# Kernel tuning notes

Measured on AMD Instinct MI355X. Metric: run time of the kernel, lower is better.

The kernel has to match this reference:

```python
import jax, jax.numpy as jnp
import numpy as np

N_NODES = 100000
N_EDGES = 1600000
D = 128


def setup_inputs() -> dict:
    key = jax.random.key(0)
    ks = jax.random.split(key, 10)
    features = jax.random.normal(ks[0], (N_NODES, D), dtype=jnp.float32)
    edge_index = jax.random.randint(ks[1], (2, N_EDGES), 0, N_NODES, dtype=jnp.int64)
    edge_weight = jax.random.uniform(ks[2], (N_EDGES,), dtype=jnp.float32)
    scale = 1.0 / np.sqrt(D)
    W1 = jax.random.normal(ks[3], (D, D), dtype=jnp.float32) * scale
    b1 = jnp.zeros((D,), dtype=jnp.float32)
    a1 = jnp.full((D,), 0.25, dtype=jnp.float32)  # PReLU init
    W2 = jax.random.normal(ks[4], (D, D), dtype=jnp.float32) * scale
    b2 = jnp.zeros((D,), dtype=jnp.float32)
    a2 = jnp.full((D,), 0.25, dtype=jnp.float32)
    return {"features": features, "edge_index": edge_index, "edge_weight": edge_weight,
            "W1": W1, "b1": b1, "a1": a1, "W2": W2, "b2": b2, "a2": a2}


def _gcn_norm(edge_index, edge_weight, n_nodes):
    # PyG GCNConv default: add self-loops (weight 1), symmetric normalization.
    src, dst = edge_index[0], edge_index[1]
    loop = jnp.arange(n_nodes, dtype=src.dtype)
    src = jnp.concatenate([src, loop])
    dst = jnp.concatenate([dst, loop])
    w = jnp.concatenate([edge_weight, jnp.ones((n_nodes,), edge_weight.dtype)])
    deg = jax.ops.segment_sum(w, dst, num_segments=n_nodes)  # in-degree (target)
    dis = jnp.where(deg > 0, jax.lax.rsqrt(deg), 0.0)
    norm = dis[src] * w * dis[dst]  # [E + N]
    return src, dst, norm


def _gcn_layer(x, W, b, src, dst, norm, n_nodes):
    h = x @ W                                 # [N, D] dense GEMM first (PyG order)
    msg = h[src] * norm[:, None]              # gather + scale, [E+N, D]
    out = jax.ops.segment_sum(msg, dst, num_segments=n_nodes)
    return out + b


def _prelu(x, a):
    return jnp.where(x >= 0, x, a * x)


def reference(features, edge_index, edge_weight, W1, b1, a1, W2, b2, a2):
    n = features.shape[0]
    src, dst, norm = _gcn_norm(edge_index, edge_weight, n)
    # dropout is identity in eval mode
    x = _prelu(_gcn_layer(features, W1, b1, src, dst, norm, n), a1)
    x = _prelu(_gcn_layer(x, W2, b2, src, dst, norm, n), a2)
    return x
```

## Files before the change

kernel.cpp:

```cpp
#include <hip/hip_runtime.h>
#include <cstdint>

#define NN 100000
#define NE 1600000
#define DD 128
#define NB 250
#define BSZ 400

typedef unsigned int uint;
typedef unsigned short ushort;
typedef unsigned long long u64;

typedef __attribute__((ext_vector_type(8))) short short8;
typedef __attribute__((ext_vector_type(4))) float floatx4;

__device__ inline uint f2bf(float f) {
    uint u = __float_as_uint(f);
    return (u + 0x7fffu + ((u >> 16) & 1u)) >> 16;
}


__global__ __launch_bounds__(256) void zero_bc(uint* __restrict__ bc) {
    if (threadIdx.x < NB) bc[threadIdx.x] = 0u;
}

__global__ __launch_bounds__(256) void bucket_hist(const int* __restrict__ dst,
                                                   uint* __restrict__ bc) {
    __shared__ uint h[NB];
    int tid = threadIdx.x;
    if (tid < NB) h[tid] = 0u;
    __syncthreads();
    int e0 = blockIdx.x * 8192 + tid;
#pragma unroll
    for (int k = 0; k < 32; ++k) {
        int e = e0 + 256 * k;
        if (e < NE) atomicAdd(&h[(uint)dst[e] / BSZ], 1u);
    }
    __syncthreads();
    if (tid < NB && h[tid]) atomicAdd(&bc[tid], h[tid]);
}

__global__ __launch_bounds__(256) void bucket_prefix(const uint* __restrict__ bc,
                                                     uint* __restrict__ bbase,
                                                     uint* __restrict__ bcur) {
    int lane = threadIdx.x;
    if (lane < 64) {
        uint v[4], s = 0;
#pragma unroll
        for (int k = 0; k < 4; ++k) {
            int i = lane * 4 + k;
            v[k] = (i < NB) ? bc[i] : 0u;
            s += v[k];
        }
        uint inc = s;
#pragma unroll
        for (int d = 1; d < 64; d <<= 1) {
            uint t = __shfl_up(inc, (unsigned)d, 64);
            if (lane >= d) inc += t;
        }
        uint run = inc - s;
#pragma unroll
        for (int k = 0; k < 4; ++k) {
            int i = lane * 4 + k;
            if (i < NB) { bbase[i] = run; bcur[i] = run; run += v[k]; }
        }
        if (lane == 63) bbase[NB] = run;
    }
}

__global__ __launch_bounds__(256) void bucket_append(const int* __restrict__ src,
                                                     const int* __restrict__ dst,
                                                     const float* __restrict__ w,
                                                     uint* __restrict__ bcur,
                                                     int2* __restrict__ etmp) {
    __shared__ uint h[NB];
    __shared__ uint res[NB];
    int tid = threadIdx.x;
    if (tid < NB) h[tid] = 0u;
    __syncthreads();
    int e0 = blockIdx.x * 4096 + tid;
    uint rank[16], bkt[16];
#pragma unroll
    for (int k = 0; k < 16; ++k) {
        int e = e0 + 256 * k;
        if (e < NE) {
            uint b = (uint)dst[e] / BSZ;
            bkt[k] = b;
            rank[k] = atomicAdd(&h[b], 1u);
        } else bkt[k] = 0xffffffffu;
    }
    __syncthreads();
    if (tid < NB) res[tid] = h[tid] ? atomicAdd(&bcur[tid], h[tid]) : 0u;
    __syncthreads();
#pragma unroll
    for (int k = 0; k < 16; ++k) {
        if (bkt[k] != 0xffffffffu) {
            int e = e0 + 256 * k;
            uint dl = (uint)dst[e] - bkt[k] * BSZ;
            uint wq = (uint)(w[e] * 8388608.0f);
            if (wq > 8388607u) wq = 8388607u;
            etmp[res[bkt[k]] + rank[k]] = make_int2(src[e], (int)((dl << 23) | wq));
        }
    }
}

__global__ __launch_bounds__(256) void bucket_build(const int2* __restrict__ etmp,
                                                    const uint* __restrict__ bbase,
                                                    float* __restrict__ dis,
                                                    int* __restrict__ hist_g,
                                                    int* __restrict__ rowstart,
                                                    int2* __restrict__ edges) {
    __shared__ u64   wc[BSZ];
    __shared__ uint  cur[BSZ];
    __shared__ float disl[BSZ];
    int tid = threadIdx.x;
    int b = blockIdx.x;
    int n0 = b * BSZ;
    for (int i = tid; i < BSZ; i += 256) wc[i] = 0ull;
    __syncthreads();
    uint base = bbase[b], end = bbase[b + 1];
    for (uint i = base + tid; i < end; i += 256) {
        uint y = (uint)etmp[i].y;
        uint dl = y >> 23;
        atomicAdd(&wc[dl], ((u64)1 << 40) | (u64)(y & 0x7fffffu));
    }
    __syncthreads();
    if (tid < 64) {
        uint v[7], s = 0;
#pragma unroll
        for (int k = 0; k < 7; ++k) {
            int i = tid * 7 + k;
            v[k] = (i < BSZ) ? (uint)(wc[i] >> 40) : 0u;
            s += v[k];
        }
        uint inc = s;
#pragma unroll
        for (int d = 1; d < 64; d <<= 1) {
            uint t = __shfl_up(inc, (unsigned)d, 64);
            if (tid >= d) inc += t;
        }
        uint run = inc - s;
#pragma unroll
        for (int k = 0; k < 7; ++k) {
            int i = tid * 7 + k;
            if (i < BSZ) { cur[i] = run; run += v[k]; }
        }
    }
    __syncthreads();
    for (int i = tid; i < BSZ; i += 256) {
        u64 v = wc[i];
        float wsum = (float)(v & 0xffffffffffull) * (1.0f / 8388608.0f);
        float ds = rsqrtf(1.0f + wsum);
        disl[i] = ds;
        dis[n0 + i] = ds;
        hist_g[n0 + i] = (int)(v >> 40);
        rowstart[n0 + i] = (int)(base + cur[i]);
    }
    __syncthreads();
    for (uint i = base + tid; i < end; i += 256) {
        int2 e = etmp[i];
        uint y = (uint)e.y;
        uint dl = y >> 23;
        float wv = (float)(y & 0x7fffffu) * (1.0f / 8388608.0f);
        uint p = atomicAdd(&cur[dl], 1u);
        float nrm = wv * disl[dl];
        edges[base + p] = make_int2(e.x, __float_as_int(nrm));
    }
}

#define WTS 136
#define NTILES ((NN + 63) / 64)

template <bool AF32>
__global__ __launch_bounds__(256) void gemm_mfma(const void* __restrict__ Xv,
                                                 const float* __restrict__ W,
                                                 const float* __restrict__ dis,
                                                 ushort* __restrict__ HB) {
    __shared__ ushort Wt[DD * WTS];
    int tid = threadIdx.x;
#pragma unroll
    for (int it = 0; it < 16; ++it) {
        int flat = (tid + it * 256) * 4;
        int k = flat >> 7, n = flat & 127;
        float4 wv = *(const float4*)&W[flat];
        Wt[(n + 0) * WTS + k] = (ushort)f2bf(wv.x);
        Wt[(n + 1) * WTS + k] = (ushort)f2bf(wv.y);
        Wt[(n + 2) * WTS + k] = (ushort)f2bf(wv.z);
        Wt[(n + 3) * WTS + k] = (ushort)f2bf(wv.w);
    }
    __syncthreads();

    int wave = tid >> 6, lane = tid & 63;
    int q = lane >> 4, l16 = lane & 15;

    for (int tile = blockIdx.x; tile < NTILES; tile += gridDim.x) {
        int row0 = tile * 64 + wave * 16;

        int arow = row0 + l16;
        if (arow >= NN) arow = NN - 1;
        short8 afr[4];
        if (AF32) {
            const float* xr = (const float*)Xv + (size_t)arow * DD + q * 8;
#pragma unroll
            for (int ks = 0; ks < 4; ++ks) {
                float4 f0 = *(const float4*)(xr + ks * 32);
                float4 f1 = *(const float4*)(xr + ks * 32 + 4);
                uint4 u;
                u.x = f2bf(f0.x) | (f2bf(f0.y) << 16);
                u.y = f2bf(f0.z) | (f2bf(f0.w) << 16);
                u.z = f2bf(f1.x) | (f2bf(f1.y) << 16);
                u.w = f2bf(f1.z) | (f2bf(f1.w) << 16);
                afr[ks] = __builtin_bit_cast(short8, u);
            }
        } else {
            const ushort* xr = (const ushort*)Xv + (size_t)arow * DD + q * 8;
#pragma unroll
            for (int ks = 0; ks < 4; ++ks)
                afr[ks] = *(const short8*)(xr + ks * 32);
        }

        floatx4 acc[8];
#pragma unroll
        for (int ct = 0; ct < 8; ++ct) acc[ct] = (floatx4)(0.0f);

#pragma unroll
        for (int ct = 0; ct < 8; ++ct) {
            const ushort* wp = &Wt[(ct * 16 + l16) * WTS + q * 8];
#pragma unroll
            for (int ks = 0; ks < 4; ++ks) {
                short8 bfr = *(const short8*)(wp + ks * 32);
                acc[ct] = __builtin_amdgcn_mfma_f32_16x16x32_bf16(afr[ks], bfr, acc[ct], 0, 0, 0);
            }
        }

#pragma unroll
        for (int reg = 0; reg < 4; ++reg) {
            int r = row0 + q * 4 + reg;
            if (r < NN) {
                float ds = dis[r];
                ushort* orow = HB + (size_t)r * DD + l16;
#pragma unroll
                for (int ct = 0; ct < 8; ++ct)
                    orow[ct * 16] = (ushort)f2bf(acc[ct][reg] * ds);
            }
        }
    }
}

__device__ inline float4 bf4(uint2 u) {
    float4 f;
    f.x = __uint_as_float(u.x << 16);
    f.y = __uint_as_float(u.x & 0xffff0000u);
    f.z = __uint_as_float(u.y << 16);
    f.w = __uint_as_float(u.y & 0xffff0000u);
    return f;
}

template <bool BF16OUT>
__global__ __launch_bounds__(256) void gather_finalize(const ushort* __restrict__ hb,
                                                       const int2* __restrict__ edges,
                                                       const int* __restrict__ rowstart,
                                                       const int* __restrict__ hist,
                                                       const float* __restrict__ dis,
                                                       const float* __restrict__ b,
                                                       const float* __restrict__ a,
                                                       void* __restrict__ xout) {
    int tid = threadIdx.x;
    int lane = tid & 31;
    int node = blockIdx.x * 8 + (tid >> 5);

    const int2* ep = edges + rowstart[node];
    int cnt = hist[node];
    float ds = dis[node];

    const uint2* hrow = (const uint2*)(hb + (size_t)node * DD) + lane;
    float4 self = bf4(*hrow);
    float4 acc0, acc1, acc2, acc3;
    acc0.x = self.x * ds; acc0.y = self.y * ds;
    acc0.z = self.z * ds; acc0.w = self.w * ds;
    acc1 = make_float4(0.f, 0.f, 0.f, 0.f);
    acc2 = make_float4(0.f, 0.f, 0.f, 0.f);
    acc3 = make_float4(0.f, 0.f, 0.f, 0.f);

    int j = 0;
    for (; j + 8 <= cnt; j += 8) {
        int2 e0 = ep[j];     int2 e1 = ep[j + 1];
        int2 e2 = ep[j + 2]; int2 e3 = ep[j + 3];
        int2 e4 = ep[j + 4]; int2 e5 = ep[j + 5];
        int2 e6 = ep[j + 6]; int2 e7 = ep[j + 7];
        uint2 u0 = *((const uint2*)(hb + (size_t)e0.x * DD) + lane);
        uint2 u1 = *((const uint2*)(hb + (size_t)e1.x * DD) + lane);
        uint2 u2 = *((const uint2*)(hb + (size_t)e2.x * DD) + lane);
        uint2 u3 = *((const uint2*)(hb + (size_t)e3.x * DD) + lane);
        uint2 u4 = *((const uint2*)(hb + (size_t)e4.x * DD) + lane);
        uint2 u5 = *((const uint2*)(hb + (size_t)e5.x * DD) + lane);
        uint2 u6 = *((const uint2*)(hb + (size_t)e6.x * DD) + lane);
        uint2 u7 = *((const uint2*)(hb + (size_t)e7.x * DD) + lane);
        float n0 = __int_as_float(e0.y), n1 = __int_as_float(e1.y);
        float n2 = __int_as_float(e2.y), n3 = __int_as_float(e3.y);
        float n4 = __int_as_float(e4.y), n5 = __int_as_float(e5.y);
        float n6 = __int_as_float(e6.y), n7 = __int_as_float(e7.y);
        float4 v0 = bf4(u0), v1 = bf4(u1), v2 = bf4(u2), v3 = bf4(u3);
        float4 v4 = bf4(u4), v5 = bf4(u5), v6 = bf4(u6), v7 = bf4(u7);
        acc0.x += v0.x * n0; acc0.y += v0.y * n0; acc0.z += v0.z * n0; acc0.w += v0.w * n0;
        acc1.x += v1.x * n1; acc1.y += v1.y * n1; acc1.z += v1.z * n1; acc1.w += v1.w * n1;
        acc2.x += v2.x * n2; acc2.y += v2.y * n2; acc2.z += v2.z * n2; acc2.w += v2.w * n2;
        acc3.x += v3.x * n3; acc3.y += v3.y * n3; acc3.z += v3.z * n3; acc3.w += v3.w * n3;
        acc0.x += v4.x * n4; acc0.y += v4.y * n4; acc0.z += v4.z * n4; acc0.w += v4.w * n4;
        acc1.x += v5.x * n5; acc1.y += v5.y * n5; acc1.z += v5.z * n5; acc1.w += v5.w * n5;
        acc2.x += v6.x * n6; acc2.y += v6.y * n6; acc2.z += v6.z * n6; acc2.w += v6.w * n6;
        acc3.x += v7.x * n7; acc3.y += v7.y * n7; acc3.z += v7.z * n7; acc3.w += v7.w * n7;
    }
    for (; j < cnt; ++j) {
        int2 e = ep[j];
        uint2 u = *((const uint2*)(hb + (size_t)e.x * DD) + lane);
        float n = __int_as_float(e.y);
        float4 v = bf4(u);
        acc0.x += v.x * n; acc0.y += v.y * n; acc0.z += v.z * n; acc0.w += v.w * n;
    }

    float4 bb = ((const float4*)b)[lane];
    float4 aa = ((const float4*)a)[lane];
    float4 r;
    r.x = acc0.x + acc1.x + acc2.x + acc3.x + bb.x;
    r.y = acc0.y + acc1.y + acc2.y + acc3.y + bb.y;
    r.z = acc0.z + acc1.z + acc2.z + acc3.z + bb.z;
    r.w = acc0.w + acc1.w + acc2.w + acc3.w + bb.w;
    r.x = r.x >= 0.f ? r.x : aa.x * r.x;
    r.y = r.y >= 0.f ? r.y : aa.y * r.y;
    r.z = r.z >= 0.f ? r.z : aa.z * r.z;
    r.w = r.w >= 0.f ? r.w : aa.w * r.w;
    if (BF16OUT) {
        uint2 o;
        o.x = f2bf(r.x) | (f2bf(r.y) << 16);
        o.y = f2bf(r.z) | (f2bf(r.w) << 16);
        ((uint2*)xout)[(size_t)node * 32 + lane] = o;
    } else {
        ((float4*)xout)[(size_t)node * 32 + lane] = r;
    }
}

extern "C" void kernel_launch(void* const* d_in, const int* in_sizes, int n_in,
                              void* d_out, int out_size, void* d_ws, size_t ws_size,
                              hipStream_t stream) {
    const float* feat = (const float*)d_in[0];
    const int*   ei   = (const int*)d_in[1];
    const float* ew   = (const float*)d_in[2];
    const float* W1   = (const float*)d_in[3];
    const float* b1   = (const float*)d_in[4];
    const float* a1   = (const float*)d_in[5];
    const float* W2   = (const float*)d_in[6];
    const float* b2   = (const float*)d_in[7];
    const float* a2   = (const float*)d_in[8];
    float* out = (float*)d_out;

    const int* srcp = ei;
    const int* dstp = ei + NE;

    char* wsb = (char*)d_ws;
    size_t off = 0;
    uint* bc     = (uint*)(wsb + off); off += 4096;
    uint* bbase  = (uint*)(wsb + off); off += 4096;
    uint* bcur   = (uint*)(wsb + off); off += 4096;
    float* dis   = (float*)(wsb + off); off += 4ull * NN;
    int* hist    = (int*)(wsb + off); off += 4ull * NN;
    int* rowstart= (int*)(wsb + off); off += 4ull * NN;
    int2* etmp   = (int2*)(wsb + off); off += 8ull * NE;
    int2* edges  = (int2*)(wsb + off); off += 8ull * NE;
    ushort* hb   = (ushort*)(wsb + off); off += 2ull * NN * DD;
    ushort* x1b  = (ushort*)(wsb + off); off += 2ull * NN * DD;

    zero_bc<<<1, 256, 0, stream>>>(bc);
    bucket_hist<<<(NE + 8191) / 8192, 256, 0, stream>>>(dstp, bc);
    bucket_prefix<<<1, 256, 0, stream>>>(bc, bbase, bcur);
    bucket_append<<<(NE + 4095) / 4096, 256, 0, stream>>>(srcp, dstp, ew, bcur, etmp);
    bucket_build<<<NB, 256, 0, stream>>>(etmp, bbase, dis, hist, rowstart, edges);

    const int gemm_blocks = (NTILES + 1) / 2;
    const int gath_blocks = NN / 8;

    gemm_mfma<true><<<gemm_blocks, 256, 0, stream>>>(feat, W1, dis, hb);
    gather_finalize<true><<<gath_blocks, 256, 0, stream>>>(hb, edges, rowstart, hist, dis, b1, a1, x1b);
    gemm_mfma<false><<<gemm_blocks, 256, 0, stream>>>(x1b, W2, dis, hb);
    gather_finalize<false><<<gath_blocks, 256, 0, stream>>>(hb, edges, rowstart, hist, dis, b2, a2, out);
}
```

Measured before the change: 379.0 us.

## Gather with one wavefront per node and lane-broadcast edge lists

Restructures the gather/finalize kernel so each node is handled by a full 64-lane wavefront that reads 4 bytes (two bf16 values) per lane, instead of a half-wave of 32 lanes reading 8 bytes each. Edge records are loaded 16 at a time, one per lane, and broadcast with readlane, so the per-edge index loads become scalar and the next chunk is prefetched. The aim is to cut redundant per-lane edge loads and raise memory-level parallelism in the bandwidth-bound gather. In exchange, each row gather is narrower per lane, twice as many blocks are launched, and tail iterations do masked dummy loads of row 0.

```diff
diff --git a/kernel.cpp b/kernel.cpp
--- a/kernel.cpp
+++ b/kernel.cpp
@@ -247,15 +247,6 @@
     }
 }
 
-__device__ inline float4 bf4(uint2 u) {
-    float4 f;
-    f.x = __uint_as_float(u.x << 16);
-    f.y = __uint_as_float(u.x & 0xffff0000u);
-    f.z = __uint_as_float(u.y << 16);
-    f.w = __uint_as_float(u.y & 0xffff0000u);
-    return f;
-}
-
 template <bool BF16OUT>
 __global__ __launch_bounds__(256) void gather_finalize(const ushort* __restrict__ hb,
                                                        const int2* __restrict__ edges,
@@ -265,78 +256,54 @@
                                                        const float* __restrict__ b,
                                                        const float* __restrict__ a,
                                                        void* __restrict__ xout) {
-    int tid = threadIdx.x;
-    int lane = tid & 31;
-    int node = blockIdx.x * 8 + (tid >> 5);
-
-    const int2* ep = edges + rowstart[node];
-    int cnt = hist[node];
+    int node = blockIdx.x * 4 + (threadIdx.x >> 6);
+    int lane = threadIdx.x & 63;
+
+    int rs  = __builtin_amdgcn_readfirstlane(rowstart[node]);
+    int cnt = __builtin_amdgcn_readfirstlane(hist[node]);
     float ds = dis[node];
-
-    const uint2* hrow = (const uint2*)(hb + (size_t)node * DD) + lane;
-    float4 self = bf4(*hrow);
-    float4 acc0, acc1, acc2, acc3;
-    acc0.x = self.x * ds; acc0.y = self.y * ds;
-    acc0.z = self.z * ds; acc0.w = self.w * ds;
-    acc1 = make_float4(0.f, 0.f, 0.f, 0.f);
-    acc2 = make_float4(0.f, 0.f, 0.f, 0.f);
-    acc3 = make_float4(0.f, 0.f, 0.f, 0.f);
-
-    int j = 0;
-    for (; j + 8 <= cnt; j += 8) {
-        int2 e0 = ep[j];     int2 e1 = ep[j + 1];
-        int2 e2 = ep[j + 2]; int2 e3 = ep[j + 3];
-        int2 e4 = ep[j + 4]; int2 e5 = ep[j + 5];
-        int2 e6 = ep[j + 6]; int2 e7 = ep[j + 7];
-        uint2 u0 = *((const uint2*)(hb + (size_t)e0.x * DD) + lane);
-        uint2 u1 = *((const uint2*)(hb + (size_t)e1.x * DD) + lane);
-        uint2 u2 = *((const uint2*)(hb + (size_t)e2.x * DD) + lane);
-        uint2 u3 = *((const uint2*)(hb + (size_t)e3.x * DD) + lane);
-        uint2 u4 = *((const uint2*)(hb + (size_t)e4.x * DD) + lane);
-        uint2 u5 = *((const uint2*)(hb + (size_t)e5.x * DD) + lane);
-        uint2 u6 = *((const uint2*)(hb + (size_t)e6.x * DD) + lane);
-        uint2 u7 = *((const uint2*)(hb + (size_t)e7.x * DD) + lane);
-        float n0 = __int_as_float(e0.y), n1 = __int_as_float(e1.y);
-        float n2 = __int_as_float(e2.y), n3 = __int_as_float(e3.y);
-        float n4 = __int_as_float(e4.y), n5 = __int_as_float(e5.y);
-        float n6 = __int_as_float(e6.y), n7 = __int_as_float(e7.y);
-        float4 v0 = bf4(u0), v1 = bf4(u1), v2 = bf4(u2), v3 = bf4(u3);
-        float4 v4 = bf4(u4), v5 = bf4(u5), v6 = bf4(u6), v7 = bf4(u7);
-        acc0.x += v0.x * n0; acc0.y += v0.y * n0; acc0.z += v0.z * n0; acc0.w += v0.w * n0;
-        acc1.x += v1.x * n1; acc1.y += v1.y * n1; acc1.z += v1.z * n1; acc1.w += v1.w * n1;
-        acc2.x += v2.x * n2; acc2.y += v2.y * n2; acc2.z += v2.z * n2; acc2.w += v2.w * n2;
-        acc3.x += v3.x * n3; acc3.y += v3.y * n3; acc3.z += v3.z * n3; acc3.w += v3.w * n3;
-        acc0.x += v4.x * n4; acc0.y += v4.y * n4; acc0.z += v4.z * n4; acc0.w += v4.w * n4;
-        acc1.x += v5.x * n5; acc1.y += v5.y * n5; acc1.z += v5.z * n5; acc1.w += v5.w * n5;
-        acc2.x += v6.x * n6; acc2.y += v6.y * n6; acc2.z += v6.z * n6; acc2.w += v6.w * n6;
-        acc3.x += v7.x * n7; acc3.y += v7.y * n7; acc3.z += v7.z * n7; acc3.w += v7.w * n7;
-    }
-    for (; j < cnt; ++j) {
-        int2 e = ep[j];
-        uint2 u = *((const uint2*)(hb + (size_t)e.x * DD) + lane);
-        float n = __int_as_float(e.y);
-        float4 v = bf4(u);
-        acc0.x += v.x * n; acc0.y += v.y * n; acc0.z += v.z * n; acc0.w += v.w * n;
-    }
-
-    float4 bb = ((const float4*)b)[lane];
-    float4 aa = ((const float4*)a)[lane];
-    float4 r;
-    r.x = acc0.x + acc1.x + acc2.x + acc3.x + bb.x;
-    r.y = acc0.y + acc1.y + acc2.y + acc3.y + bb.y;
-    r.z = acc0.z + acc1.z + acc2.z + acc3.z + bb.z;
-    r.w = acc0.w + acc1.w + acc2.w + acc3.w + bb.w;
-    r.x = r.x >= 0.f ? r.x : aa.x * r.x;
-    r.y = r.y >= 0.f ? r.y : aa.y * r.y;
-    r.z = r.z >= 0.f ? r.z : aa.z * r.z;
-    r.w = r.w >= 0.f ? r.w : aa.w * r.w;
+    const int2* ep = edges + rs;
+    const uint* hrows = (const uint*)hb;
+
+    uint su = hrows[(size_t)node * 64 + lane];
+    float2 acc0, acc1, acc2, acc3;
+    acc0.x = __uint_as_float(su << 16) * ds;
+    acc0.y = __uint_as_float(su & 0xffff0000u) * ds;
+    acc1 = make_float2(0.f, 0.f);
+    acc2 = make_float2(0.f, 0.f);
+    acc3 = make_float2(0.f, 0.f);
+
+    int nb = (cnt + 15) >> 4;
+    int2 cur = ep[lane & 15];
+    for (int t = 0; t < nb; ++t) {
+        int2 nxt = ep[(t + 1) * 16 + (lane & 15)];
+        int rem = cnt - t * 16;
+#pragma unroll
+        for (int k = 0; k < 16; ++k) {
+            uint sidx = (uint)__builtin_amdgcn_readlane(cur.x, k);
+            uint nrmu = (uint)__builtin_amdgcn_readlane(cur.y, k);
+            bool live = k < rem;
+            sidx = live ? sidx : 0u;
+            float nrm = live ? __uint_as_float(nrmu) : 0.0f;
+            uint v = hrows[(size_t)sidx * 64 + lane];
+            float2* ac = (k & 3) == 0 ? &acc0 : (k & 3) == 1 ? &acc1 : (k & 3) == 2 ? &acc2 : &acc3;
+            ac->x += __uint_as_float(v << 16) * nrm;
+            ac->y += __uint_as_float(v & 0xffff0000u) * nrm;
+        }
+        cur = nxt;
+    }
+
+    float2 bb = ((const float2*)b)[lane];
+    float2 aa = ((const float2*)a)[lane];
+    float r0 = acc0.x + acc1.x + acc2.x + acc3.x + bb.x;
+    float r1 = acc0.y + acc1.y + acc2.y + acc3.y + bb.y;
+    r0 = r0 >= 0.f ? r0 : aa.x * r0;
+    r1 = r1 >= 0.f ? r1 : aa.y * r1;
     if (BF16OUT) {
-        uint2 o;
-        o.x = f2bf(r.x) | (f2bf(r.y) << 16);
-        o.y = f2bf(r.z) | (f2bf(r.w) << 16);
-        ((uint2*)xout)[(size_t)node * 32 + lane] = o;
+        ((uint*)xout)[(size_t)node * 64 + lane] = f2bf(r0) | (f2bf(r1) << 16);
     } else {
-        ((float4*)xout)[(size_t)node * 32 + lane] = r;
+        float2 o; o.x = r0; o.y = r1;
+        ((float2*)xout)[(size_t)node * 64 + lane] = o;
     }
 }
 
@@ -377,7 +344,7 @@
     bucket_build<<<NB, 256, 0, stream>>>(etmp, bbase, dis, hist, rowstart, edges);
 
     const int gemm_blocks = (NTILES + 1) / 2;
-    const int gath_blocks = NN / 8;
+    const int gath_blocks = NN / 4;
 
     gemm_mfma<true><<<gemm_blocks, 256, 0, stream>>>(feat, W1, dis, hb);
     gather_finalize<true><<<gath_blocks, 256, 0, stream>>>(hb, edges, rowstart, hist, dis, b1, a1, x1b);
```

Result: faster. 359.3 us (-5.2%).
